# Kernel optimization log

Hardware: AMD Instinct MI355X
Metric: run time of the kernel (lower is better)

The kernel has to match this reference:

```python
import jax, jax.numpy as jnp
import numpy as np

EPS = 0.001  # additive floor applied after relu, as in the torch code


def setup_inputs() -> dict:
    key = jax.random.key(0)
    kA, kB, kW = jax.random.split(key, 3)
    M, N, C, H, W = 512, 64, 128, 8, 8
    A = jax.random.normal(kA, (M, C, H, W), dtype=jnp.float32)
    B = jax.random.normal(kB, (N, C, H, W), dtype=jnp.float32)
    Wg = jax.random.normal(kW, (C, C), dtype=jnp.float32) * 0.01  # Wg.data.normal_(0.0, 0.01)
    return {"A": A, "B": B, "Wg": Wg}


def reference(A, B, Wg):
    # Faithful vectorization of MIMOcom.get_source_dst_max(A, B, dir=True).
    # Torch loops i,j over HxW: B0 = B[:, i, j, :]; G = B0 @ Wg;
    # combination[m, n, p] = sum_c A[m, p, c] * G[n, c]; running max over (i, j).
    M, C, H, W = A.shape
    N = B.shape[0]
    P = H * W
    Af = jnp.transpose(A, (0, 2, 3, 1)).reshape(M, P, C)  # [M, P, C]
    Bf = jnp.transpose(B, (0, 2, 3, 1)).reshape(N, P, C)  # [N, Q, C]
    G = Bf @ Wg                                           # [N, Q, D]
    scores = jnp.einsum('mpd,nqd->mnpq', Af, G)           # [M, N, P, Q]
    comb_max = scores.max(axis=-1)                        # max over B positions q
    return jax.nn.relu(comb_max) + EPS                    # [M, N, P]
```

## Files before the change

kernel.cpp:

```cpp
#include <hip/hip_runtime.h>
#include <hip/hip_bf16.h>
#include <stdint.h>

typedef __attribute__((ext_vector_type(8))) short bf16x8;
typedef __attribute__((ext_vector_type(16))) float f32x16;
using bf16 = __hip_bfloat16;

static constexpr int Mdim = 512;
static constexpr int Ndim = 64;
static constexpr int Cdim = 128;
static constexpr int Pdim = 64;
static constexpr float EPS_ADD = 0.001f;

__device__ __forceinline__ void gll16(const void* gsrc, void* ldst) {
    const __attribute__((address_space(1))) unsigned int* g =
        (const __attribute__((address_space(1))) unsigned int*)gsrc;
    __attribute__((address_space(3))) unsigned int* l =
        (__attribute__((address_space(3))) unsigned int*)(uintptr_t)ldst;
    __builtin_amdgcn_global_load_lds(g, l, 16, 0, 0);
}

__global__ void prep_kernel(const float* __restrict__ A, const float* __restrict__ B,
                            const float* __restrict__ Wg,
                            bf16* __restrict__ Afrag, bf16* __restrict__ Gfrag) {
    __shared__ float lds[128 * 65];
    const int t = threadIdx.x;

    if (blockIdx.x < 512) {
        const int m = blockIdx.x;
        const float* __restrict__ Am = A + (size_t)m * (Cdim * Pdim);
#pragma unroll
        for (int i = 0; i < 8; ++i) {
            int v = t + i * 256;
            int gidx = v * 4;
            int c = gidx >> 6, p = gidx & 63;
            float4 val = *reinterpret_cast<const float4*>(Am + gidx);
            float* dst = &lds[c * 65 + p];
            dst[0] = val.x; dst[1] = val.y; dst[2] = val.z; dst[3] = val.w;
        }
        __syncthreads();

        unsigned* __restrict__ dst32 = (unsigned*)(Afrag + (size_t)m * 8192);
#pragma unroll
        for (int i = 0; i < 16; ++i) {
            int pr = t + i * 256;
            int p = pr >> 6;
            int c = (pr & 63) << 1;
            float f0 = lds[c * 65 + p];
            float f1 = lds[(c + 1) * 65 + p];
            union { bf16 hh[2]; unsigned u; } pk;
            pk.hh[0] = __float2bfloat16(f0);
            pk.hh[1] = __float2bfloat16(f1);
            int h = p >> 5, l31 = p & 31;
            int ks = c >> 4, hi = (c >> 3) & 1, e = c & 7;
            dst32[h * 2048 + ks * 256 + hi * 128 + l31 * 4 + (e >> 1)] = pk.u;
        }
    } else {
        const int nb = blockIdx.x - 512;
        const int n  = nb >> 2;
        const int q0 = (nb & 3) * 16;
        const float* __restrict__ Bn = B + (size_t)n * (Cdim * Pdim);
#pragma unroll
        for (int i = 0; i < 8; ++i) {
            int v = t + i * 256;
            int gidx = v * 4;
            int c = gidx >> 6, q = gidx & 63;
            float4 val = *reinterpret_cast<const float4*>(Bn + gidx);
            float* dst = &lds[c * 65 + q];
            dst[0] = val.x; dst[1] = val.y; dst[2] = val.z; dst[3] = val.w;
        }
        __syncthreads();

        const int d  = t & 127;
        const int qb = q0 + (t >> 7) * 8;
        float acc[8] = {0.f, 0.f, 0.f, 0.f, 0.f, 0.f, 0.f, 0.f};
        for (int c = 0; c < 128; ++c) {
            float w = Wg[c * 128 + d];
#pragma unroll
            for (int qi = 0; qi < 8; ++qi)
                acc[qi] = fmaf(lds[c * 65 + qb + qi], w, acc[qi]);
        }
        bf16* __restrict__ gdst = Gfrag + (size_t)n * 8192;
        const int ks = d >> 4, hi = (d >> 3) & 1, e = d & 7;
#pragma unroll
        for (int qi = 0; qi < 8; ++qi) {
            int q = qb + qi;
            int qt = q >> 5, l31 = q & 31;
            gdst[qt * 4096 + ks * 512 + hi * 256 + l31 * 8 + e] = __float2bfloat16(acc[qi]);
        }
    }
}

__global__ __launch_bounds__(512, 2)
void gemm_max_kernel(const bf16* __restrict__ Afrag, const bf16* __restrict__ Gfrag,
                     float* __restrict__ out) {
    __shared__ bf16 sG[4][8192];
    const int tid  = threadIdx.x;
    const int lane = tid & 63;
    const int wv   = tid >> 6;
    const int mi = wv >> 1, h = wv & 1;
    const int l31 = lane & 31, hi = lane >> 5;
    const int mg = blockIdx.x & 63;
    const int bn = blockIdx.x >> 6;
    const int m0 = mg * 8 + mi * 2;

    bf16x8 a[2][8];
#pragma unroll
    for (int u = 0; u < 2; ++u) {
        const bf16* Ap = Afrag + (size_t)(m0 + u) * 8192 + h * 4096 + lane * 8;
#pragma unroll
        for (int ks = 0; ks < 8; ++ks)
            a[u][ks] = *reinterpret_cast<const bf16x8*>(Ap + ks * 512);
    }
    {
        const char* Gsrc = (const char*)(Gfrag + (size_t)(bn * 4) * 8192);
#pragma unroll
        for (int i = 0; i < 8; ++i) {
            int f = (i * 512 + tid) * 16;
            gll16(Gsrc + f, (char*)sG + f);
        }
    }
    asm volatile("s_waitcnt vmcnt(0)" ::: "memory");
    __builtin_amdgcn_s_barrier();
    __builtin_amdgcn_sched_barrier(0);

    const f32x16 z16 = {0.f,0.f,0.f,0.f,0.f,0.f,0.f,0.f,0.f,0.f,0.f,0.f,0.f,0.f,0.f,0.f};
    f32x16 acc0, acc1;
    bf16x8 gf0[8], gf1[8];

    auto ldgf = [&](bf16x8 (&g)[8], const char* base) {
#pragma unroll
        for (int ks = 0; ks < 8; ++ks)
            g[ks] = *reinterpret_cast<const bf16x8*>(base + ks * 1024);
    };
    auto mmcl = [&](const bf16x8 (&gf)[8]) {
        acc0 = __builtin_amdgcn_mfma_f32_32x32x16_bf16(gf[0], a[0][0], z16, 0, 0, 0);
        acc1 = __builtin_amdgcn_mfma_f32_32x32x16_bf16(gf[0], a[1][0], z16, 0, 0, 0);
#pragma unroll
        for (int ks = 1; ks < 8; ++ks) {
            acc0 = __builtin_amdgcn_mfma_f32_32x32x16_bf16(gf[ks], a[0][ks], acc0, 0, 0, 0);
            acc1 = __builtin_amdgcn_mfma_f32_32x32x16_bf16(gf[ks], a[1][ks], acc1, 0, 0, 0);
        }
    };
    auto red16 = [&](const f32x16& v) -> float {
        float x0 = fmaxf(v[0], v[1]),  x1 = fmaxf(v[2], v[3]);
        float x2 = fmaxf(v[4], v[5]),  x3 = fmaxf(v[6], v[7]);
        float x4 = fmaxf(v[8], v[9]),  x5 = fmaxf(v[10], v[11]);
        float x6 = fmaxf(v[12], v[13]), x7 = fmaxf(v[14], v[15]);
        x0 = fmaxf(x0, x1); x2 = fmaxf(x2, x3);
        x4 = fmaxf(x4, x5); x6 = fmaxf(x6, x7);
        return fmaxf(fmaxf(x0, x2), fmaxf(x4, x6));
    };

#pragma unroll
    for (int s = 0; s < 4; ++s) {
        const char* gb = (const char*)sG + s * 16384 + lane * 16;
        ldgf(gf0, gb);
        ldgf(gf1, gb + 8192);
        mmcl(gf0);
        float t0 = red16(acc0), t1 = red16(acc1);
        mmcl(gf1);
        t0 = fmaxf(t0, red16(acc0));
        t1 = fmaxf(t1, red16(acc1));
        t0 = fmaxf(t0, __shfl_xor(t0, 32));
        t1 = fmaxf(t1, __shfl_xor(t1, 32));
        const int n = bn * 4 + s;
        const float sv = hi ? t1 : t0;
        out[(size_t)(m0 + hi) * 4096 + n * 64 + h * 32 + l31] =
            fmaxf(sv, 0.f) + EPS_ADD;
    }
}

extern "C" void kernel_launch(void* const* d_in, const int* in_sizes, int n_in,
                              void* d_out, int out_size, void* d_ws, size_t ws_size,
                              hipStream_t stream) {
    const float* A  = (const float*)d_in[0];
    const float* B  = (const float*)d_in[1];
    const float* Wg = (const float*)d_in[2];
    float* out = (float*)d_out;

    bf16* Afrag = (bf16*)d_ws;
    bf16* Gfrag = (bf16*)((char*)d_ws + (size_t)Mdim * Pdim * Cdim * sizeof(bf16));

    prep_kernel<<<768, 256, 0, stream>>>(A, B, Wg, Afrag, Gfrag);
    gemm_max_kernel<<<1024, 512, 0, stream>>>(Afrag, Gfrag, out);
}
```

Before: 48.27 us.

## Give each wave four A rows so every LDS G fragment feeds four MFMAs

The GEMM-max kernel now runs 4 waves of 256 threads instead of 8, and each wave holds four m rows of A in registers instead of two. Each G fragment read from LDS is reused across four MFMAs, which halves LDS traffic per MFMA. The G tile is still staged once per block. In exchange, occupancy drops (launch bounds 256,1), register pressure rises from holding four A fragment sets and four accumulators, and each block has fewer waves to hide latency.

New measurement: 49.48 us. 1.02x slower.

```diff
diff --git a/kernel.cpp b/kernel.cpp
--- a/kernel.cpp
+++ b/kernel.cpp
@@ -91,7 +91,17 @@
     }
 }
 
-__global__ __launch_bounds__(512, 2)
+__device__ __forceinline__ float red16(const f32x16& v) {
+    float x0 = fmaxf(v[0], v[1]),  x1 = fmaxf(v[2], v[3]);
+    float x2 = fmaxf(v[4], v[5]),  x3 = fmaxf(v[6], v[7]);
+    float x4 = fmaxf(v[8], v[9]),  x5 = fmaxf(v[10], v[11]);
+    float x6 = fmaxf(v[12], v[13]), x7 = fmaxf(v[14], v[15]);
+    x0 = fmaxf(x0, x1); x2 = fmaxf(x2, x3);
+    x4 = fmaxf(x4, x5); x6 = fmaxf(x6, x7);
+    return fmaxf(fmaxf(x0, x2), fmaxf(x4, x6));
+}
+
+__global__ __launch_bounds__(256, 1)
 void gemm_max_kernel(const bf16* __restrict__ Afrag, const bf16* __restrict__ Gfrag,
                      float* __restrict__ out) {
     __shared__ bf16 sG[4][8192];
@@ -102,21 +112,25 @@
     const int l31 = lane & 31, hi = lane >> 5;
     const int mg = blockIdx.x & 63;
     const int bn = blockIdx.x >> 6;
-    const int m0 = mg * 8 + mi * 2;
+    const int m0 = mg * 8 + mi * 4;
 
-    bf16x8 a[2][8];
+    bf16x8 a0[8], a1[8], a2[8], a3[8];
+    {
+        const bf16* Ap = Afrag + (size_t)m0 * 8192 + h * 4096 + lane * 8;
 #pragma unroll
-    for (int u = 0; u < 2; ++u) {
-        const bf16* Ap = Afrag + (size_t)(m0 + u) * 8192 + h * 4096 + lane * 8;
+        for (int ks = 0; ks < 8; ++ks) a0[ks] = *reinterpret_cast<const bf16x8*>(Ap + ks * 512);
 #pragma unroll
-        for (int ks = 0; ks < 8; ++ks)
-            a[u][ks] = *reinterpret_cast<const bf16x8*>(Ap + ks * 512);
+        for (int ks = 0; ks < 8; ++ks) a1[ks] = *reinterpret_cast<const bf16x8*>(Ap + 8192 + ks * 512);
+#pragma unroll
+        for (int ks = 0; ks < 8; ++ks) a2[ks] = *reinterpret_cast<const bf16x8*>(Ap + 16384 + ks * 512);
+#pragma unroll
+        for (int ks = 0; ks < 8; ++ks) a3[ks] = *reinterpret_cast<const bf16x8*>(Ap + 24576 + ks * 512);
     }
     {
         const char* Gsrc = (const char*)(Gfrag + (size_t)(bn * 4) * 8192);
 #pragma unroll
-        for (int i = 0; i < 8; ++i) {
-            int f = (i * 512 + tid) * 16;
+        for (int i = 0; i < 16; ++i) {
+            int f = (i * 256 + tid) * 16;
             gll16(Gsrc + f, (char*)sG + f);
         }
     }
@@ -125,49 +139,38 @@
     __builtin_amdgcn_sched_barrier(0);
 
     const f32x16 z16 = {0.f,0.f,0.f,0.f,0.f,0.f,0.f,0.f,0.f,0.f,0.f,0.f,0.f,0.f,0.f,0.f};
-    f32x16 acc0, acc1;
-    bf16x8 gf0[8], gf1[8];
-
-    auto ldgf = [&](bf16x8 (&g)[8], const char* base) {
-#pragma unroll
-        for (int ks = 0; ks < 8; ++ks)
-            g[ks] = *reinterpret_cast<const bf16x8*>(base + ks * 1024);
-    };
-    auto mmcl = [&](const bf16x8 (&gf)[8]) {
-        acc0 = __builtin_amdgcn_mfma_f32_32x32x16_bf16(gf[0], a[0][0], z16, 0, 0, 0);
-        acc1 = __builtin_amdgcn_mfma_f32_32x32x16_bf16(gf[0], a[1][0], z16, 0, 0, 0);
-#pragma unroll
-        for (int ks = 1; ks < 8; ++ks) {
-            acc0 = __builtin_amdgcn_mfma_f32_32x32x16_bf16(gf[ks], a[0][ks], acc0, 0, 0, 0);
-            acc1 = __builtin_amdgcn_mfma_f32_32x32x16_bf16(gf[ks], a[1][ks], acc1, 0, 0, 0);
-        }
-    };
-    auto red16 = [&](const f32x16& v) -> float {
-        float x0 = fmaxf(v[0], v[1]),  x1 = fmaxf(v[2], v[3]);
-        float x2 = fmaxf(v[4], v[5]),  x3 = fmaxf(v[6], v[7]);
-        float x4 = fmaxf(v[8], v[9]),  x5 = fmaxf(v[10], v[11]);
-        float x6 = fmaxf(v[12], v[13]), x7 = fmaxf(v[14], v[15]);
-        x0 = fmaxf(x0, x1); x2 = fmaxf(x2, x3);
-        x4 = fmaxf(x4, x5); x6 = fmaxf(x6, x7);
-        return fmaxf(fmaxf(x0, x2), fmaxf(x4, x6));
-    };
 
 #pragma unroll
     for (int s = 0; s < 4; ++s) {
         const char* gb = (const char*)sG + s * 16384 + lane * 16;
-        ldgf(gf0, gb);
-        ldgf(gf1, gb + 8192);
-        mmcl(gf0);
-        float t0 = red16(acc0), t1 = red16(acc1);
-        mmcl(gf1);
-        t0 = fmaxf(t0, red16(acc0));
-        t1 = fmaxf(t1, red16(acc1));
-        t0 = fmaxf(t0, __shfl_xor(t0, 32));
-        t1 = fmaxf(t1, __shfl_xor(t1, 32));
+        float r0, r1, r2, r3;
+#pragma unroll
+        for (int qt = 0; qt < 2; ++qt) {
+            f32x16 acc0, acc1, acc2, acc3;
+#pragma unroll
+            for (int ks = 0; ks < 8; ++ks) {
+                bf16x8 gf = *reinterpret_cast<const bf16x8*>(gb + qt * 8192 + ks * 1024);
+                acc0 = __builtin_amdgcn_mfma_f32_32x32x16_bf16(gf, a0[ks], ks == 0 ? z16 : acc0, 0, 0, 0);
+                acc1 = __builtin_amdgcn_mfma_f32_32x32x16_bf16(gf, a1[ks], ks == 0 ? z16 : acc1, 0, 0, 0);
+                acc2 = __builtin_amdgcn_mfma_f32_32x32x16_bf16(gf, a2[ks], ks == 0 ? z16 : acc2, 0, 0, 0);
+                acc3 = __builtin_amdgcn_mfma_f32_32x32x16_bf16(gf, a3[ks], ks == 0 ? z16 : acc3, 0, 0, 0);
+            }
+            float t0 = red16(acc0), t1 = red16(acc1);
+            float t2 = red16(acc2), t3 = red16(acc3);
+            if (qt == 0) { r0 = t0; r1 = t1; r2 = t2; r3 = t3; }
+            else { r0 = fmaxf(r0, t0); r1 = fmaxf(r1, t1);
+                   r2 = fmaxf(r2, t2); r3 = fmaxf(r3, t3); }
+        }
+        r0 = fmaxf(r0, __shfl_xor(r0, 32));
+        r1 = fmaxf(r1, __shfl_xor(r1, 32));
+        r2 = fmaxf(r2, __shfl_xor(r2, 32));
+        r3 = fmaxf(r3, __shfl_xor(r3, 32));
         const int n = bn * 4 + s;
-        const float sv = hi ? t1 : t0;
-        out[(size_t)(m0 + hi) * 4096 + n * 64 + h * 32 + l31] =
-            fmaxf(sv, 0.f) + EPS_ADD;
+        const float sa = hi ? r2 : r0;
+        const float sb = hi ? r3 : r1;
+        float* ob = out + (size_t)(m0 + hi * 2) * 4096 + n * 64 + h * 32 + l31;
+        ob[0]    = fmaxf(sa, 0.f) + EPS_ADD;
+        ob[4096] = fmaxf(sb, 0.f) + EPS_ADD;
     }
 }
 
@@ -183,5 +186,5 @@
     bf16* Gfrag = (bf16*)((char*)d_ws + (size_t)Mdim * Pdim * Cdim * sizeof(bf16));
 
     prep_kernel<<<768, 256, 0, stream>>>(A, B, Wg, Afrag, Gfrag);
-    gemm_max_kernel<<<1024, 512, 0, stream>>>(Afrag, Gfrag, out);
+    gemm_max_kernel<<<1024, 256, 0, stream>>>(Afrag, Gfrag, out);
 }
```
